# Performance work log

Measured on AMD Instinct MI355X. Metric: run time of the kernel, lower is better.

Reference implementation:

```python
import jax, jax.numpy as jnp
import numpy as np

R_TBR = 0.5
P_BASE = 50.0
ALPHA = 100.0
H_BASELINE = 0.0
T_AMBIENT = -10.0
EPS = 1e-8


def _ternary_quantize(weight):
    gamma = jnp.mean(jnp.abs(weight))
    # round-half-to-even matches torch.round
    return jnp.clip(jnp.round(weight / (gamma + EPS)), -1.0, 1.0)


def _entropy_3bin(w_q):
    n = w_q.size
    # histc(bins=3, min=-1, max=1) on values in {-1,0,1} -> exact bin counts
    counts = jnp.stack([
        jnp.sum(w_q == -1.0),
        jnp.sum(w_q == 0.0),
        jnp.sum(w_q == 1.0),
    ]).astype(jnp.float32)
    p = counts / n
    # -sum p*log2 p over p>0 (jnp.where keeps it jit-safe)
    return -jnp.sum(jnp.where(p > 0, p * jnp.log2(jnp.where(p > 0, p, 1.0)), 0.0))


def setup_inputs() -> dict:
    key = jax.random.key(0)
    k1, k2 = jax.random.split(key)
    x = jax.random.normal(k1, (8192, 4096), dtype=jnp.float32)
    weight = jax.random.normal(k2, (4096, 4096), dtype=jnp.float32)  # [out, in]
    return {"x": x, "weight": weight}


def reference(x, weight):
    w_q = _ternary_quantize(weight)            # ternary {-1,0,1}, shape [out, in]
    entropy = _entropy_3bin(w_q)
    heat_flux = ALPHA * jax.nn.relu(entropy - H_BASELINE)
    q_total = P_BASE + heat_flux
    t_current = T_AMBIENT + q_total * R_TBR    # guardrail value (no overload at T_ambient=-10)
    output = x @ w_q.T                         # F.linear(x, W_q), [N, out]
    return (output, t_current, entropy)
```

## Files before the change

### kernel.cpp

```cpp
#include <hip/hip_runtime.h>
#include <stdint.h>

typedef short bf16x8 __attribute__((ext_vector_type(8)));
typedef float f32x4 __attribute__((ext_vector_type(4)));

#define M_ROWS 8192
#define N_OUT  4096
#define K_DIM  4096
#define NW     16777216.0

__device__ __forceinline__ void gload16(const void* g, void* l) {
    __builtin_amdgcn_global_load_lds((const __attribute__((address_space(1))) void*)g,
                                     (__attribute__((address_space(3))) void*)l,
                                     16, 0, 0);
}

__device__ __forceinline__ unsigned short f2bf(float f) {
    unsigned u = __float_as_uint(f);
    unsigned r = 0x7FFFu + ((u >> 16) & 1u);
    return (unsigned short)((u + r) >> 16);
}

__global__ __launch_bounds__(256) void k_gamma(const float* __restrict__ w,
                                               double* __restrict__ sum) {
    const int n4 = (K_DIM * N_OUT) / 4;
    int idx = blockIdx.x * blockDim.x + threadIdx.x;
    int stride = gridDim.x * blockDim.x;
    const float4* w4 = (const float4*)w;
    double local = 0.0;
    for (int i = idx; i < n4; i += stride) {
        float4 v = w4[i];
        local += (double)fabsf(v.x) + (double)fabsf(v.y) +
                 (double)fabsf(v.z) + (double)fabsf(v.w);
    }
    __shared__ double sm[256];
    sm[threadIdx.x] = local;
    __syncthreads();
    for (int s = 128; s > 0; s >>= 1) {
        if (threadIdx.x < s) sm[threadIdx.x] += sm[threadIdx.x + s];
        __syncthreads();
    }
    if (threadIdx.x == 0) atomicAdd(sum, sm[0]);
}

__global__ __launch_bounds__(256) void k_quant(const float* __restrict__ w,
                                               const double* __restrict__ sum,
                                               unsigned short* __restrict__ wq,
                                               unsigned int* __restrict__ counts,
                                               int do_store) {
    const float gamma = (float)(*sum / NW);
    const float denom = gamma + 1e-8f;
    const int n4 = (K_DIM * N_OUT) / 4;
    int idx = blockIdx.x * blockDim.x + threadIdx.x;
    int stride = gridDim.x * blockDim.x;
    const float4* w4 = (const float4*)w;
    unsigned cm = 0, cp = 0;
    for (int i = idx; i < n4; i += stride) {
        float4 v = w4[i];
        float q0 = fminf(1.f, fmaxf(-1.f, rintf(v.x / denom)));
        float q1 = fminf(1.f, fmaxf(-1.f, rintf(v.y / denom)));
        float q2 = fminf(1.f, fmaxf(-1.f, rintf(v.z / denom)));
        float q3 = fminf(1.f, fmaxf(-1.f, rintf(v.w / denom)));
        cm += (q0 < -0.5f) + (q1 < -0.5f) + (q2 < -0.5f) + (q3 < -0.5f);
        cp += (q0 >  0.5f) + (q1 >  0.5f) + (q2 >  0.5f) + (q3 >  0.5f);
        if (do_store) {
            unsigned b0 = (q0 < -0.5f) ? 0xBF80u : (q0 > 0.5f ? 0x3F80u : 0u);
            unsigned b1 = (q1 < -0.5f) ? 0xBF80u : (q1 > 0.5f ? 0x3F80u : 0u);
            unsigned b2 = (q2 < -0.5f) ? 0xBF80u : (q2 > 0.5f ? 0x3F80u : 0u);
            unsigned b3 = (q3 < -0.5f) ? 0xBF80u : (q3 > 0.5f ? 0x3F80u : 0u);
            uint2 pk;
            pk.x = b0 | (b1 << 16);
            pk.y = b2 | (b3 << 16);
            ((uint2*)wq)[i] = pk;
        }
    }
    __shared__ unsigned smc[512];
    smc[threadIdx.x] = cm;
    smc[256 + threadIdx.x] = cp;
    __syncthreads();
    for (int s = 128; s > 0; s >>= 1) {
        if (threadIdx.x < s) {
            smc[threadIdx.x] += smc[threadIdx.x + s];
            smc[256 + threadIdx.x] += smc[256 + threadIdx.x + s];
        }
        __syncthreads();
    }
    if (threadIdx.x == 0) {
        atomicAdd(&counts[0], smc[0]);
        atomicAdd(&counts[1], smc[256]);
    }
}

__global__ __launch_bounds__(256) void k_cvt(const float* __restrict__ x,
                                             unsigned short* __restrict__ xb) {
    const int n4 = (M_ROWS * K_DIM) / 4;
    int idx = blockIdx.x * blockDim.x + threadIdx.x;
    int stride = gridDim.x * blockDim.x;
    const float4* x4 = (const float4*)x;
    for (int i = idx; i < n4; i += stride) {
        float4 v = x4[i];
        uint2 pk;
        pk.x = (unsigned)f2bf(v.x) | ((unsigned)f2bf(v.y) << 16);
        pk.y = (unsigned)f2bf(v.z) | ((unsigned)f2bf(v.w) << 16);
        ((uint2*)xb)[i] = pk;
    }
}

__global__ void k_fin(const unsigned int* __restrict__ counts,
                      float* __restrict__ outs) {
    double n = NW;
    double c1 = (double)counts[0];
    double c2 = (double)counts[1];
    double c0 = n - c1 - c2;
    double H = 0.0;
    if (c1 > 0.0) { double p = c1 / n; H -= p * log2(p); }
    if (c0 > 0.0) { double p = c0 / n; H -= p * log2(p); }
    if (c2 > 0.0) { double p = c2 / n; H -= p * log2(p); }
    float Hf = (float)H;
    float heat = 100.0f * fmaxf(Hf, 0.0f);
    outs[0] = -10.0f + (50.0f + heat) * 0.5f;
    outs[1] = Hf;
}


__device__ __forceinline__ void stage_half(const unsigned short* __restrict__ A,
                                           const unsigned short* __restrict__ B,
                                           char* lds, int H, int tm, int tn,
                                           int tid) {
    const int kt = H >> 2;
    const int q  = H & 3;
    const unsigned short* src = (q & 2) ? B : A;
    const int rb = ((q & 2) ? tn : tm) * 256 + (q & 1) * 128;
    const int row = rb + ((tid >> 6) << 4) + (tid & 15);
    const unsigned short* g0 = src + (size_t)row * K_DIM + kt * 64 + ((tid >> 4) & 3) * 8;
    char* d = lds + ((size_t)(kt & 1) << 16) + (q << 14) + tid * 16;
    gload16(g0, d);
    gload16(g0 + 32, d + 8192);
}

#define MFMA_QUAD(ACCM, ACCN, AF, BF)                                          \
    __builtin_amdgcn_s_barrier();                                              \
    asm volatile("s_waitcnt lgkmcnt(0)" ::: "memory");                         \
    __builtin_amdgcn_s_setprio(1);                                             \
    _Pragma("unroll") for (int mm = 0; mm < 4; ++mm)                           \
    _Pragma("unroll") for (int nn = 0; nn < 2; ++nn)                           \
    _Pragma("unroll") for (int ks = 0; ks < 2; ++ks)                           \
        acc[(ACCM) + mm][(ACCN) + nn] = __builtin_amdgcn_mfma_f32_16x16x32_bf16( \
            AF[mm][ks], BF[nn][ks], acc[(ACCM) + mm][(ACCN) + nn], 0, 0, 0);   \
    __builtin_amdgcn_s_setprio(0);

__global__ __launch_bounds__(512, 2) void k_gemm2(const unsigned short* __restrict__ A,
                                                  const unsigned short* __restrict__ B,
                                                  float* __restrict__ C) {
    extern __shared__ char smem[];
    const int tid  = threadIdx.x;
    const int lane = tid & 63;
    const int wid  = tid >> 6;
    const int wr   = wid >> 2;
    const int wc   = wid & 3;
    const int fr   = lane & 15;
    const int khi  = lane >> 4;

    const int lin = blockIdx.x;
    const int s   = (lin & 7) * 64 + (lin >> 3);
    const int tm  = s & 31;
    const int tn  = s >> 5;

    f32x4 acc[8][4] = {};

    stage_half(A, B, smem, 0, tm, tn, tid);
    stage_half(A, B, smem, 1, tm, tn, tid);
    stage_half(A, B, smem, 2, tm, tn, tid);
    stage_half(A, B, smem, 3, tm, tn, tid);
    stage_half(A, B, smem, 6, tm, tn, tid);
    stage_half(A, B, smem, 7, tm, tn, tid);
    asm volatile("s_waitcnt vmcnt(0)" ::: "memory");
    __builtin_amdgcn_s_barrier();

    bf16x8 afr[4][2], b0[2][2], b1[2][2];
    const int bsel = (wc & 1) * 4;

    for (int tau = 0; tau < 64; ++tau) {
        const char* aptr = smem + ((size_t)(tau & 1) << 16) + ((size_t)wr << 14) + lane * 16;
        const char* bptr = smem + ((size_t)(tau & 1) << 16) + 32768 + ((size_t)(wc >> 1) << 14)
                         + bsel * 1024 + lane * 16;
        const int g = tau * 4;

#pragma unroll
        for (int mm = 0; mm < 4; ++mm)
#pragma unroll
            for (int ks = 0; ks < 2; ++ks)
                afr[mm][ks] = *(const bf16x8*)(aptr + (ks * 8 + mm) * 1024);
#pragma unroll
        for (int nn = 0; nn < 2; ++nn)
#pragma unroll
            for (int ks = 0; ks < 2; ++ks)
                b0[nn][ks] = *(const bf16x8*)(bptr + (ks * 8 + nn) * 1024);
        if (g + 4 < 256) stage_half(A, B, smem, g + 4, tm, tn, tid);
        MFMA_QUAD(0, 0, afr, b0)
        __builtin_amdgcn_s_barrier();

#pragma unroll
        for (int nn = 0; nn < 2; ++nn)
#pragma unroll
            for (int ks = 0; ks < 2; ++ks)
                b1[nn][ks] = *(const bf16x8*)(bptr + (ks * 8 + 2 + nn) * 1024);
        if (g + 5 < 256) stage_half(A, B, smem, g + 5, tm, tn, tid);
        MFMA_QUAD(0, 2, afr, b1)
        __builtin_amdgcn_s_barrier();

#pragma unroll
        for (int mm = 0; mm < 4; ++mm)
#pragma unroll
            for (int ks = 0; ks < 2; ++ks)
                afr[mm][ks] = *(const bf16x8*)(aptr + (ks * 8 + 4 + mm) * 1024);
        if (g + 10 < 256) stage_half(A, B, smem, g + 10, tm, tn, tid);
        MFMA_QUAD(4, 2, afr, b1)
        __builtin_amdgcn_s_barrier();

        if (g + 11 < 256) stage_half(A, B, smem, g + 11, tm, tn, tid);
        MFMA_QUAD(4, 0, afr, b0)
        if (tau < 62) {
            asm volatile("s_waitcnt vmcnt(4)" ::: "memory");
        } else {
            asm volatile("s_waitcnt vmcnt(0)" ::: "memory");
        }
        __builtin_amdgcn_s_barrier();
    }

    const size_t crow = (size_t)(tm * 256 + wr * 128 + khi * 4);
    const int    ccol = tn * 256 + wc * 64 + fr;
#pragma unroll
    for (int m = 0; m < 8; ++m)
#pragma unroll
        for (int n = 0; n < 4; ++n) {
            float* cp = C + (crow + m * 16) * N_OUT + (ccol + n * 16);
#pragma unroll
            for (int j = 0; j < 4; ++j)
                cp[(size_t)j * N_OUT] = acc[m][n][j];
        }
}

__global__ __launch_bounds__(256) void fb_gemm(const float* __restrict__ X,
                                               const float* __restrict__ W,
                                               const double* __restrict__ sum,
                                               float* __restrict__ C) {
    __shared__ float Xs[64][33];
    __shared__ float Ws[64][33];
    const float gamma = (float)(*sum / NW);
    const float denom = gamma + 1e-8f;
    const int tid = threadIdx.x;
    const int bm = blockIdx.y * 64;
    const int bn = blockIdx.x * 64;
    const int tr = tid >> 4, tc = tid & 15;
    const int lrow = tid >> 2;
    const int lcol = (tid & 3) * 8;
    float acc[4][4] = {};
    for (int k0 = 0; k0 < K_DIM; k0 += 32) {
        const float4* xs = (const float4*)(X + (size_t)(bm + lrow) * K_DIM + k0 + lcol);
        float4 v0 = xs[0], v1 = xs[1];
        Xs[lrow][lcol + 0] = v0.x; Xs[lrow][lcol + 1] = v0.y;
        Xs[lrow][lcol + 2] = v0.z; Xs[lrow][lcol + 3] = v0.w;
        Xs[lrow][lcol + 4] = v1.x; Xs[lrow][lcol + 5] = v1.y;
        Xs[lrow][lcol + 6] = v1.z; Xs[lrow][lcol + 7] = v1.w;
        const float4* wsrc = (const float4*)(W + (size_t)(bn + lrow) * K_DIM + k0 + lcol);
        float4 w0 = wsrc[0], w1 = wsrc[1];
        Ws[lrow][lcol + 0] = fminf(1.f, fmaxf(-1.f, rintf(w0.x / denom)));
        Ws[lrow][lcol + 1] = fminf(1.f, fmaxf(-1.f, rintf(w0.y / denom)));
        Ws[lrow][lcol + 2] = fminf(1.f, fmaxf(-1.f, rintf(w0.z / denom)));
        Ws[lrow][lcol + 3] = fminf(1.f, fmaxf(-1.f, rintf(w0.w / denom)));
        Ws[lrow][lcol + 4] = fminf(1.f, fmaxf(-1.f, rintf(w1.x / denom)));
        Ws[lrow][lcol + 5] = fminf(1.f, fmaxf(-1.f, rintf(w1.y / denom)));
        Ws[lrow][lcol + 6] = fminf(1.f, fmaxf(-1.f, rintf(w1.z / denom)));
        Ws[lrow][lcol + 7] = fminf(1.f, fmaxf(-1.f, rintf(w1.w / denom)));
        __syncthreads();
#pragma unroll 8
        for (int kk = 0; kk < 32; ++kk) {
            float a0 = Xs[tr * 4 + 0][kk], a1 = Xs[tr * 4 + 1][kk];
            float a2 = Xs[tr * 4 + 2][kk], a3 = Xs[tr * 4 + 3][kk];
            float b0 = Ws[tc * 4 + 0][kk], b1 = Ws[tc * 4 + 1][kk];
            float b2 = Ws[tc * 4 + 2][kk], b3 = Ws[tc * 4 + 3][kk];
            acc[0][0] += a0 * b0; acc[0][1] += a0 * b1; acc[0][2] += a0 * b2; acc[0][3] += a0 * b3;
            acc[1][0] += a1 * b0; acc[1][1] += a1 * b1; acc[1][2] += a1 * b2; acc[1][3] += a1 * b3;
            acc[2][0] += a2 * b0; acc[2][1] += a2 * b1; acc[2][2] += a2 * b2; acc[2][3] += a2 * b3;
            acc[3][0] += a3 * b0; acc[3][1] += a3 * b1; acc[3][2] += a3 * b2; acc[3][3] += a3 * b3;
        }
        __syncthreads();
    }
#pragma unroll
    for (int i = 0; i < 4; ++i)
#pragma unroll
        for (int j = 0; j < 4; ++j)
            C[(size_t)(bm + tr * 4 + i) * N_OUT + (bn + tc * 4 + j)] = acc[i][j];
}

extern "C" void kernel_launch(void* const* d_in, const int* in_sizes, int n_in,
                              void* d_out, int out_size, void* d_ws, size_t ws_size,
                              hipStream_t stream) {
    (void)in_sizes; (void)n_in; (void)out_size;
    const float* x = (const float*)d_in[0];
    const float* w = (const float*)d_in[1];
    float* out = (float*)d_out;
    float* scalars = out + (size_t)M_ROWS * N_OUT;

    double* sum = (double*)d_ws;
    unsigned int* counts = (unsigned int*)((char*)d_ws + 8);
    unsigned short* xb = (unsigned short*)((char*)d_ws + 64);
    unsigned short* wq = (unsigned short*)((char*)d_ws + 64 + (size_t)M_ROWS * K_DIM * 2);

    const size_t need = 64 + (size_t)M_ROWS * K_DIM * 2 + (size_t)N_OUT * K_DIM * 2;
    const int fast = (ws_size >= need);

    hipMemsetAsync(d_ws, 0, 16, stream);
    k_gamma<<<1024, 256, 0, stream>>>(w, sum);

    if (fast) {
        k_cvt<<<2048, 256, 0, stream>>>(x, xb);
        k_quant<<<1024, 256, 0, stream>>>(w, sum, wq, counts, 1);
        k_fin<<<1, 1, 0, stream>>>(counts, scalars);
        hipFuncSetAttribute(reinterpret_cast<const void*>(k_gemm2),
                            hipFuncAttributeMaxDynamicSharedMemorySize, 131072);
        k_gemm2<<<dim3(512), 512, 131072, stream>>>(xb, wq, out);
    } else {
        k_quant<<<1024, 256, 0, stream>>>(w, sum, nullptr, counts, 0);
        k_fin<<<1, 1, 0, stream>>>(counts, scalars);
        dim3 grid(N_OUT / 64, M_ROWS / 64);
        fb_gemm<<<grid, 256, 0, stream>>>(x, w, sum, out);
    }
}
```

Before: 370.4 us.

## Restructure GEMM inner loop into k-half phases with full-N fragments

```diff
diff --git a/kernel.cpp b/kernel.cpp
--- a/kernel.cpp
+++ b/kernel.cpp
@@ -138,15 +138,14 @@
     gload16(g0 + 32, d + 8192);
 }
 
-#define MFMA_QUAD(ACCM, ACCN, AF, BF)                                          \
-    __builtin_amdgcn_s_barrier();                                              \
+#define MFMA_PH(MH, AF, BF)                                                    \
     asm volatile("s_waitcnt lgkmcnt(0)" ::: "memory");                         \
+    __builtin_amdgcn_sched_barrier(0);                                         \
     __builtin_amdgcn_s_setprio(1);                                             \
     _Pragma("unroll") for (int mm = 0; mm < 4; ++mm)                           \
-    _Pragma("unroll") for (int nn = 0; nn < 2; ++nn)                           \
-    _Pragma("unroll") for (int ks = 0; ks < 2; ++ks)                           \
-        acc[(ACCM) + mm][(ACCN) + nn] = __builtin_amdgcn_mfma_f32_16x16x32_bf16( \
-            AF[mm][ks], BF[nn][ks], acc[(ACCM) + mm][(ACCN) + nn], 0, 0, 0);   \
+    _Pragma("unroll") for (int nn = 0; nn < 4; ++nn)                           \
+        acc[(MH)*4 + mm][nn] = __builtin_amdgcn_mfma_f32_16x16x32_bf16(        \
+            AF[mm], BF[nn], acc[(MH)*4 + mm][nn], 0, 0, 0);                    \
     __builtin_amdgcn_s_setprio(0);
 
 __global__ __launch_bounds__(512, 2) void k_gemm2(const unsigned short* __restrict__ A,
@@ -177,7 +176,7 @@
     asm volatile("s_waitcnt vmcnt(0)" ::: "memory");
     __builtin_amdgcn_s_barrier();
 
-    bf16x8 afr[4][2], b0[2][2], b1[2][2];
+    bf16x8 afr0[4], afr1[4], bk0[4], bk1[4];
     const int bsel = (wc & 1) * 4;
 
     for (int tau = 0; tau < 64; ++tau) {
@@ -188,38 +187,36 @@
 
 #pragma unroll
         for (int mm = 0; mm < 4; ++mm)
-#pragma unroll
-            for (int ks = 0; ks < 2; ++ks)
-                afr[mm][ks] = *(const bf16x8*)(aptr + (ks * 8 + mm) * 1024);
-#pragma unroll
-        for (int nn = 0; nn < 2; ++nn)
-#pragma unroll
-            for (int ks = 0; ks < 2; ++ks)
-                b0[nn][ks] = *(const bf16x8*)(bptr + (ks * 8 + nn) * 1024);
+            afr0[mm] = *(const bf16x8*)(aptr + (0 * 8 + mm) * 1024);
+#pragma unroll
+        for (int nn = 0; nn < 4; ++nn)
+            bk0[nn] = *(const bf16x8*)(bptr + (0 * 8 + nn) * 1024);
         if (g + 4 < 256) stage_half(A, B, smem, g + 4, tm, tn, tid);
-        MFMA_QUAD(0, 0, afr, b0)
+        MFMA_PH(0, afr0, bk0)
         __builtin_amdgcn_s_barrier();
 
 #pragma unroll
-        for (int nn = 0; nn < 2; ++nn)
-#pragma unroll
-            for (int ks = 0; ks < 2; ++ks)
-                b1[nn][ks] = *(const bf16x8*)(bptr + (ks * 8 + 2 + nn) * 1024);
+        for (int mm = 0; mm < 4; ++mm)
+            afr1[mm] = *(const bf16x8*)(aptr + (1 * 8 + mm) * 1024);
+#pragma unroll
+        for (int nn = 0; nn < 4; ++nn)
+            bk1[nn] = *(const bf16x8*)(bptr + (1 * 8 + nn) * 1024);
         if (g + 5 < 256) stage_half(A, B, smem, g + 5, tm, tn, tid);
-        MFMA_QUAD(0, 2, afr, b1)
+        MFMA_PH(0, afr1, bk1)
         __builtin_amdgcn_s_barrier();
 
 #pragma unroll
         for (int mm = 0; mm < 4; ++mm)
-#pragma unroll
-            for (int ks = 0; ks < 2; ++ks)
-                afr[mm][ks] = *(const bf16x8*)(aptr + (ks * 8 + 4 + mm) * 1024);
+            afr0[mm] = *(const bf16x8*)(aptr + (0 * 8 + 4 + mm) * 1024);
         if (g + 10 < 256) stage_half(A, B, smem, g + 10, tm, tn, tid);
-        MFMA_QUAD(4, 2, afr, b1)
+        MFMA_PH(1, afr0, bk0)
         __builtin_amdgcn_s_barrier();
 
+#pragma unroll
+        for (int mm = 0; mm < 4; ++mm)
+            afr1[mm] = *(const bf16x8*)(aptr + (1 * 8 + 4 + mm) * 1024);
         if (g + 11 < 256) stage_half(A, B, smem, g + 11, tm, tn, tid);
-        MFMA_QUAD(4, 0, afr, b0)
+        MFMA_PH(1, afr1, bk1)
         if (tau < 62) {
             asm volatile("s_waitcnt vmcnt(4)" ::: "memory");
         } else {
```

Measured after the change: 371.5 us. About the same (+0.3%).
